# Performance work log

Measured on AMD Instinct MI355X. Metric: run time of the kernel, lower is better.

## Reference

```python
import jax, jax.numpy as jnp
import numpy as np

B, S, H = 64, 512, 1024
HID = 512
EPS = 1e-5


def setup_inputs() -> dict:
    key = jax.random.key(0)
    ks = jax.random.split(key, 10)
    bert_outputs = jax.random.normal(ks[0], (B, S, H), dtype=jnp.float32)
    # offsets: [A_start, A_end, B_start, B_end, pron_idx]; spans need start<=end
    pa = jnp.sort(jax.random.randint(ks[1], (B, 2), 0, S), axis=1)
    pb = jnp.sort(jax.random.randint(ks[2], (B, 2), 0, S), axis=1)
    pron = jax.random.randint(ks[3], (B, 1), 0, S)
    offsets = jnp.concatenate([pa, pb, pron], axis=1).astype(jnp.int64)
    W1 = jax.random.normal(ks[4], (3 * H, HID), dtype=jnp.float32) * 0.02
    b1 = jnp.zeros((HID,), dtype=jnp.float32)
    gamma = jnp.ones((HID,), dtype=jnp.float32)
    beta = jnp.zeros((HID,), dtype=jnp.float32)
    running_mean = jax.random.normal(ks[5], (HID,), dtype=jnp.float32) * 0.1
    running_var = jax.random.uniform(ks[6], (HID,), dtype=jnp.float32) + 0.5
    W2 = jax.random.normal(ks[7], (HID, 3), dtype=jnp.float32) * 0.02
    b2 = jnp.zeros((3,), dtype=jnp.float32)
    return {"bert_outputs": bert_outputs, "offsets": offsets, "W1": W1, "b1": b1,
            "gamma": gamma, "beta": beta, "running_mean": running_mean,
            "running_var": running_var, "W2": W2, "b2": b2}


def _span_mean(bert, start, end):
    # bert: [B,S,H]; start/end: [B] inclusive span -> masked mean over S
    pos = jnp.arange(bert.shape[1])  # [S]
    mask = ((pos >= start[:, None]) & (pos <= end[:, None])).astype(bert.dtype)  # [B,S]
    return jnp.einsum('bs,bsh->bh', mask, bert) / mask.sum(axis=1, keepdims=True)


def reference(bert_outputs, offsets, W1, b1, gamma, beta, running_mean, running_var, W2, b2):
    emb_a = _span_mean(bert_outputs, offsets[:, 0], offsets[:, 1])
    emb_b = _span_mean(bert_outputs, offsets[:, 2], offsets[:, 3])
    emb_p = bert_outputs[jnp.arange(bert_outputs.shape[0]), offsets[:, 4]]  # [B,H]
    x = jnp.concatenate([emb_a, emb_b, emb_p], axis=1)  # [B,3H]
    # Dropout is identity in eval mode
    h = x @ W1 + b1
    # BatchNorm1d (eval mode, running stats)
    h = (h - running_mean) * jax.lax.rsqrt(running_var + EPS) * gamma + beta
    h = jnp.where(h >= 0, h, 0.01 * h)  # LeakyReLU(0.01)
    return h @ W2 + b2
```

## Files before the change

kernel.cpp:

```cpp
#include <hip/hip_runtime.h>
#include <hip/hip_bf16.h>

#define B 64
#define S 512
#define H 1024
#define HID 512
#define EPS 1e-5f

__global__ __launch_bounds__(1024) void span_kernel(
    const float* __restrict__ bert, const int* __restrict__ offsets,
    float* __restrict__ x) {
    const int b  = blockIdx.x;
    const int e  = blockIdx.y;
    const int tx = threadIdx.x;
    const int ty = threadIdx.y;

    int start, end;
    if (e == 0)      { start = offsets[b * 5 + 0]; end = offsets[b * 5 + 1]; }
    else if (e == 1) { start = offsets[b * 5 + 2]; end = offsets[b * 5 + 3]; }
    else             { start = offsets[b * 5 + 4]; end = start; }

    float4 acc = make_float4(0.f, 0.f, 0.f, 0.f);
    const size_t brow = (size_t)b * S;
    for (int s = start + ty; s <= end; s += 4) {
        const float4 v = *reinterpret_cast<const float4*>(
            bert + (brow + (size_t)s) * H + tx * 4);
        acc.x += v.x; acc.y += v.y; acc.z += v.z; acc.w += v.w;
    }

    __shared__ float4 red[4][256];
    red[ty][tx] = acc;
    __syncthreads();

    if (ty == 0) {
        float4 a0 = red[0][tx], a1 = red[1][tx], a2 = red[2][tx], a3 = red[3][tx];
        const float inv = 1.0f / (float)(end - start + 1);
        float4 r;
        r.x = (a0.x + a1.x + a2.x + a3.x) * inv;
        r.y = (a0.y + a1.y + a2.y + a3.y) * inv;
        r.z = (a0.z + a1.z + a2.z + a3.z) * inv;
        r.w = (a0.w + a1.w + a2.w + a3.w) * inv;
        *reinterpret_cast<float4*>(x + (size_t)b * (3 * H) + e * H + tx * 4) = r;
    }
}

#define KCH 192
__global__ __launch_bounds__(256) void gemm1_kernel(
    const float* __restrict__ x, const float* __restrict__ W1,
    float* __restrict__ h) {
    const int jg = threadIdx.x & 15;
    const int mg = threadIdx.x >> 4;
    const int jbase = blockIdx.x * 64 + jg * 4;
    const int kbase = blockIdx.y * KCH;

    float acc[4][4];
#pragma unroll
    for (int i = 0; i < 4; ++i)
#pragma unroll
        for (int j = 0; j < 4; ++j) acc[i][j] = 0.f;

    const int m0 = mg * 4;
    for (int k = kbase; k < kbase + KCH; k += 4) {
        float4 wv[4];
#pragma unroll
        for (int kc = 0; kc < 4; ++kc)
            wv[kc] = *reinterpret_cast<const float4*>(W1 + (size_t)(k + kc) * HID + jbase);
        float4 xv[4];
#pragma unroll
        for (int mi = 0; mi < 4; ++mi)
            xv[mi] = *reinterpret_cast<const float4*>(x + (size_t)(m0 + mi) * (3 * H) + k);
#pragma unroll
        for (int mi = 0; mi < 4; ++mi) {
            acc[mi][0] += xv[mi].x * wv[0].x + xv[mi].y * wv[1].x + xv[mi].z * wv[2].x + xv[mi].w * wv[3].x;
            acc[mi][1] += xv[mi].x * wv[0].y + xv[mi].y * wv[1].y + xv[mi].z * wv[2].y + xv[mi].w * wv[3].y;
            acc[mi][2] += xv[mi].x * wv[0].z + xv[mi].y * wv[1].z + xv[mi].z * wv[2].z + xv[mi].w * wv[3].z;
            acc[mi][3] += xv[mi].x * wv[0].w + xv[mi].y * wv[1].w + xv[mi].z * wv[2].w + xv[mi].w * wv[3].w;
        }
    }

#pragma unroll
    for (int mi = 0; mi < 4; ++mi)
#pragma unroll
        for (int ji = 0; ji < 4; ++ji)
            atomicAdd(&h[(size_t)(m0 + mi) * HID + jbase + ji], acc[mi][ji]);
}

__global__ __launch_bounds__(256) void head_kernel(
    const float* __restrict__ h, const float* __restrict__ b1,
    const float* __restrict__ gamma, const float* __restrict__ beta,
    const float* __restrict__ rm, const float* __restrict__ rv,
    const float* __restrict__ W2, const float* __restrict__ b2,
    float* __restrict__ out) {
    const int b = blockIdx.x;
    const int t = threadIdx.x;

    float c0 = 0.f, c1 = 0.f, c2 = 0.f;
    for (int j = t; j < HID; j += 256) {
        float v = (h[(size_t)b * HID + j] + b1[j] - rm[j]) * rsqrtf(rv[j] + EPS) * gamma[j] + beta[j];
        v = (v >= 0.f) ? v : 0.01f * v;
        c0 += v * W2[j * 3 + 0];
        c1 += v * W2[j * 3 + 1];
        c2 += v * W2[j * 3 + 2];
    }
#pragma unroll
    for (int off = 32; off > 0; off >>= 1) {
        c0 += __shfl_down(c0, off);
        c1 += __shfl_down(c1, off);
        c2 += __shfl_down(c2, off);
    }
    __shared__ float red[4][3];
    const int lane = t & 63, w = t >> 6;
    if (lane == 0) { red[w][0] = c0; red[w][1] = c1; red[w][2] = c2; }
    __syncthreads();
    if (t == 0) {
        out[b * 3 + 0] = red[0][0] + red[1][0] + red[2][0] + red[3][0] + b2[0];
        out[b * 3 + 1] = red[0][1] + red[1][1] + red[2][1] + red[3][1] + b2[1];
        out[b * 3 + 2] = red[0][2] + red[1][2] + red[2][2] + red[3][2] + b2[2];
    }
}

extern "C" void kernel_launch(void* const* d_in, const int* in_sizes, int n_in,
                              void* d_out, int out_size, void* d_ws, size_t ws_size,
                              hipStream_t stream) {
    const float* bert    = (const float*)d_in[0];
    const int*   offsets = (const int*)d_in[1];
    const float* W1      = (const float*)d_in[2];
    const float* b1      = (const float*)d_in[3];
    const float* gamma   = (const float*)d_in[4];
    const float* beta    = (const float*)d_in[5];
    const float* rm      = (const float*)d_in[6];
    const float* rv      = (const float*)d_in[7];
    const float* W2      = (const float*)d_in[8];
    const float* b2      = (const float*)d_in[9];
    float* out = (float*)d_out;

    float* x = (float*)d_ws;
    float* h = (float*)((char*)d_ws + (size_t)B * 3 * H * 4);

    hipMemsetAsync(h, 0, (size_t)B * HID * sizeof(float), stream);

    dim3 g1(B, 3), t1(256, 4);
    span_kernel<<<g1, t1, 0, stream>>>(bert, offsets, x);

    dim3 g2(HID / 64, (3 * H) / KCH), t2(256);
    gemm1_kernel<<<g2, t2, 0, stream>>>(x, W1, h);

    head_kernel<<<B, 256, 0, stream>>>(h, b1, gamma, beta, rm, rv, W2, b2, out);
}
```

Before: 287.6 us.

## Split span reduction across sequence chunks with atomic accumulation

The span-mean kernel now launches a third grid dimension over 64-row chunks of the sequence. Each block sums only its overlap with the span and atomically adds the scaled partial mean into x, which is now zeroed by a larger memset. The original grid had only 192 blocks, each looping serially over long spans, so this is meant to expose more parallelism for the memory-bound reduction. The cost is float atomics, a bigger memset, many empty blocks that exit early, and a summation order that is no longer deterministic.

```diff
diff --git a/kernel.cpp b/kernel.cpp
--- a/kernel.cpp
+++ b/kernel.cpp
@@ -6,42 +6,41 @@
 #define H 1024
 #define HID 512
 #define EPS 1e-5f
+#define SCHUNK 64
+#define NCH (S / SCHUNK)
 
-__global__ __launch_bounds__(1024) void span_kernel(
+__global__ __launch_bounds__(256) void span_kernel(
     const float* __restrict__ bert, const int* __restrict__ offsets,
     float* __restrict__ x) {
-    const int b  = blockIdx.x;
-    const int e  = blockIdx.y;
-    const int tx = threadIdx.x;
-    const int ty = threadIdx.y;
+    const int b = blockIdx.x;
+    const int e = blockIdx.y;
+    const int c = blockIdx.z;
 
     int start, end;
     if (e == 0)      { start = offsets[b * 5 + 0]; end = offsets[b * 5 + 1]; }
     else if (e == 1) { start = offsets[b * 5 + 2]; end = offsets[b * 5 + 3]; }
     else             { start = offsets[b * 5 + 4]; end = start; }
 
+    const int lo = max(start, c * SCHUNK);
+    const int hi = min(end, c * SCHUNK + SCHUNK - 1);
+    if (lo > hi) return;
+
+    const float inv = 1.0f / (float)(end - start + 1);
+    const int tx = threadIdx.x;
+
     float4 acc = make_float4(0.f, 0.f, 0.f, 0.f);
-    const size_t brow = (size_t)b * S;
-    for (int s = start + ty; s <= end; s += 4) {
-        const float4 v = *reinterpret_cast<const float4*>(
-            bert + (brow + (size_t)s) * H + tx * 4);
+    const float* p = bert + ((size_t)b * S + lo) * H + tx * 4;
+#pragma unroll 4
+    for (int s = lo; s <= hi; ++s, p += H) {
+        const float4 v = *reinterpret_cast<const float4*>(p);
         acc.x += v.x; acc.y += v.y; acc.z += v.z; acc.w += v.w;
     }
 
-    __shared__ float4 red[4][256];
-    red[ty][tx] = acc;
-    __syncthreads();
-
-    if (ty == 0) {
-        float4 a0 = red[0][tx], a1 = red[1][tx], a2 = red[2][tx], a3 = red[3][tx];
-        const float inv = 1.0f / (float)(end - start + 1);
-        float4 r;
-        r.x = (a0.x + a1.x + a2.x + a3.x) * inv;
-        r.y = (a0.y + a1.y + a2.y + a3.y) * inv;
-        r.z = (a0.z + a1.z + a2.z + a3.z) * inv;
-        r.w = (a0.w + a1.w + a2.w + a3.w) * inv;
-        *reinterpret_cast<float4*>(x + (size_t)b * (3 * H) + e * H + tx * 4) = r;
-    }
+    float* xp = x + (size_t)b * (3 * H) + e * H + tx * 4;
+    atomicAdd(xp + 0, acc.x * inv);
+    atomicAdd(xp + 1, acc.y * inv);
+    atomicAdd(xp + 2, acc.z * inv);
+    atomicAdd(xp + 3, acc.w * inv);
 }
 
 #define KCH 192
@@ -137,9 +136,9 @@
     float* x = (float*)d_ws;
     float* h = (float*)((char*)d_ws + (size_t)B * 3 * H * 4);
 
-    hipMemsetAsync(h, 0, (size_t)B * HID * sizeof(float), stream);
+    hipMemsetAsync(d_ws, 0, (size_t)(B * 3 * H + B * HID) * sizeof(float), stream);
 
-    dim3 g1(B, 3), t1(256, 4);
+    dim3 g1(B, 3, NCH), t1(256);
     span_kernel<<<g1, t1, 0, stream>>>(bert, offsets, x);
 
     dim3 g2(HID / 64, (3 * H) / KCH), t2(256);
```

Result: faster. 254.0 us (-11.7%).
